# Optimization experiments

Measured on AMD Instinct MI355X. Metric: run time of the kernel, lower is better.

## Reference

```python
import jax, jax.numpy as jnp
import numpy as np

N = 64  # periodic element grid per side; nnode = N^3, ndof = 3*N^3
OFFSETS = [(0,0,0),(1,0,0),(0,1,0),(1,1,0),(0,0,1),(1,0,1),(0,1,1),(1,1,1)]


def setup_inputs() -> dict:
    key = jax.random.key(0)
    k1, k2, k3 = jax.random.split(key, 3)
    ndof = 3 * N ** 3
    U = jax.random.normal(k1, (ndof,), jnp.float32)
    rho = jax.random.uniform(k2, (N, N, N), jnp.float32)
    # nodIdx [nel, 8]: the 8 corner nodes of each element with periodic wrap
    idx = np.arange(N)
    I, J, K = np.meshgrid(idx, idx, idx, indexing='ij')
    cols = []
    for (di, dj, dk) in OFFSETS:
        n = (((I + di) % N) * N + (J + dj) % N) * N + (K + dk) % N
        cols.append(n.reshape(-1))
    nodIdx = jnp.asarray(np.stack(cols, axis=1), jnp.int32)  # [nel, 8]
    # 256 element stiffness matrices (24x24, symmetric), one per H8 type code
    filters = jax.random.normal(k3, (256, 24, 24), jnp.float32) * 0.05
    filters = 0.5 * (filters + filters.transpose(0, 2, 1))
    # typeFilter: 2x2x2 powers-of-two kernel encoding corner occupancy pattern
    typeFilter = jnp.asarray((2.0 ** np.arange(8)).reshape(2, 2, 2), jnp.float32)
    return {"U": U, "rho": rho, "nodIdx": nodIdx, "filters": filters, "typeFilter": typeFilter}


def _typeH8(rho, typeFilter):
    # binarize density and compute per-element type code via periodic 2x2x2 conv
    rb = (rho > 0.5).astype(rho.dtype)
    t = jnp.zeros_like(rho)
    for (di, dj, dk) in OFFSETS:
        t = t + typeFilter[di, dj, dk] * jnp.roll(rb, shift=(-di, -dj, -dk), axis=(0, 1, 2))
    return jax.lax.stop_gradient(t).astype(jnp.int32).reshape(-1)  # [nel] in 0..255


def reference(U, rho, nodIdx, filters, typeFilter):
    types = _typeH8(rho, typeFilter)                       # [nel]
    # dof indices per element: 8 nodes x 3 dofs, periodic wrap baked into nodIdx
    dofIdx = (nodIdx.astype(jnp.int32)[:, :, None] * 3 + jnp.arange(3, dtype=jnp.int32)).reshape(-1, 24)
    Ue = U[dofIdx]                                         # [nel, 24] gather
    Ke = filters[types]                                    # [nel, 24, 24] type-conditional filter select
    KUe = jnp.einsum('eij,ej->ei', Ke, Ue)                 # element-local stiffness apply
    KU = jnp.zeros_like(U).at[dofIdx.reshape(-1)].add(KUe.reshape(-1))  # scatter-add assembly
    return KU
```

## Files before the change

kernel.cpp:

```cpp
#include <hip/hip_runtime.h>
#include <hip/hip_fp16.h>

#define NGRID 64
#define NEL (NGRID*NGRID*NGRID)
#define IDX(i,j,k) ((((i)*64 + (j)) * 64) + (k))

#define NSLAB    16
#define SLAB_EL  16384
#define NTYPE    256
#define SLAB_PAD 32768
#define PADTOT   (NSLAB*SLAB_PAD)
#define NSLOT    (PADTOT/64)
#define SLAB_SLOTS (SLAB_PAD/64)

#define WS_U4     0
#define WS_KUE    (WS_U4 + (size_t)NEL*16)
#define WS_SORTED (WS_KUE + (size_t)NEL*64)
#define WS_TYPES  (WS_SORTED + (size_t)PADTOT*4)
#define WS_BHIST  (WS_TYPES + NEL)
#define WS_SLOT   (WS_BHIST + 4096*16*4)
#define WS_NEEDED (size_t)(WS_SLOT + NSLOT*4)

__device__ __forceinline__ int type_of(const float* __restrict__ rho, int i, int j, int k) {
    int i1 = (i + 1) & 63, j1 = (j + 1) & 63, k1 = (k + 1) & 63;
    int t = 0;
    t |= (rho[IDX(i,  j,  k )] > 0.5f ? 1 : 0) << 0;
    t |= (rho[IDX(i1, j,  k )] > 0.5f ? 1 : 0) << 4;
    t |= (rho[IDX(i,  j1, k )] > 0.5f ? 1 : 0) << 2;
    t |= (rho[IDX(i1, j1, k )] > 0.5f ? 1 : 0) << 6;
    t |= (rho[IDX(i,  j,  k1)] > 0.5f ? 1 : 0) << 1;
    t |= (rho[IDX(i1, j,  k1)] > 0.5f ? 1 : 0) << 5;
    t |= (rho[IDX(i,  j1, k1)] > 0.5f ? 1 : 0) << 3;
    t |= (rho[IDX(i1, j1, k1)] > 0.5f ? 1 : 0) << 7;
    return t;
}

__global__ __launch_bounds__(1024) void k1_hist(
    const float* __restrict__ U, const float* __restrict__ rho,
    float4* __restrict__ U4, unsigned char* __restrict__ types,
    int* __restrict__ bhist)
{
    __shared__ int lh[NTYPE];
    int tid = threadIdx.x;
    int b = blockIdx.x;
    int slab = b & 15, inner = b >> 4;
    if (tid < NTYPE) lh[tid] = 0;
    __syncthreads();

    int e = slab * SLAB_EL + inner * 1024 + tid;
    U4[e] = make_float4(U[3*e + 0], U[3*e + 1], U[3*e + 2], 0.0f);
    int k = e & 63, j = (e >> 6) & 63, i = (e >> 12) & 63;
    int t = type_of(rho, i, j, k);
    types[e] = (unsigned char)t;
    atomicAdd(&lh[t], 1);
    __syncthreads();
    if (tid < NTYPE) bhist[(slab * NTYPE + tid) * 16 + inner] = lh[tid];
}

__global__ __launch_bounds__(256) void k2_scan(
    int* __restrict__ bhist, int* __restrict__ slotinfo)
{
    int slab = blockIdx.x, t = threadIdx.x;
    int base = (slab * NTYPE + t) * 16;
    int c[16], sum = 0;
    #pragma unroll
    for (int in = 0; in < 16; ++in) { c[in] = bhist[base + in]; sum += c[in]; }
    int padded = (sum + 63) & ~63;

    __shared__ int s[256];
    __shared__ int used;
    s[t] = padded;
    __syncthreads();
    #pragma unroll
    for (int off = 1; off < 256; off <<= 1) {
        int tmp = (t >= off) ? s[t - off] : 0;
        __syncthreads();
        s[t] += tmp;
        __syncthreads();
    }
    int excl = s[t] - padded;
    int run = slab * SLAB_PAD + excl;
    #pragma unroll
    for (int in = 0; in < 16; ++in) { bhist[base + in] = run; run += c[in]; }

    int slot0 = slab * SLAB_SLOTS + (excl >> 6);
    int nslots = padded >> 6;
    for (int q = 0; q < nslots; ++q) {
        int cq = sum - (q << 6);
        cq = cq > 64 ? 64 : cq;
        slotinfo[slot0 + q] = (cq << 8) | t;
    }
    if (t == 255) used = s[255] >> 6;
    __syncthreads();
    for (int q = used + t; q < SLAB_SLOTS; q += 256)
        slotinfo[slab * SLAB_SLOTS + q] = 0;
}

__global__ __launch_bounds__(1024) void k3_scatter(
    const unsigned char* __restrict__ types, const int* __restrict__ bhist,
    int* __restrict__ sorted)
{
    __shared__ int lh[NTYPE];
    int tid = threadIdx.x;
    int b = blockIdx.x;
    int slab = b & 15, inner = b >> 4;
    if (tid < NTYPE) lh[tid] = 0;
    __syncthreads();
    int e = slab * SLAB_EL + inner * 1024 + tid;
    int t = types[e];
    int rank = atomicAdd(&lh[t], 1);
    int pos = bhist[(slab * NTYPE + t) * 16 + inner] + rank;
    sorted[pos] = e;
}

__global__ __launch_bounds__(256) void k4_apply(
    const float4* __restrict__ U4, const float* __restrict__ filters,
    const int* __restrict__ sorted, const int* __restrict__ slotinfo,
    float4* __restrict__ KUe16)
{
    int b = blockIdx.x;
    int hi = b >> 3;
    int slab = (b & 7) + 8 * (hi >> 7);
    int inner = hi & 127;
    int p = slab * SLAB_PAD + inner * 256 + threadIdx.x;

    int slot = __builtin_amdgcn_readfirstlane(p >> 6);
    int packed = slotinfo[slot];
    int t   = packed & 255;
    int cnt = packed >> 8;
    const float* __restrict__ F = filters + t * 576;

    if ((int)(threadIdx.x & 63) < cnt) {
        int e = sorted[p];
        int k = e & 63, j = (e >> 6) & 63, i = (e >> 12) & 63;
        int i1 = (i + 1) & 63, j1 = (j + 1) & 63, k1 = (k + 1) & 63;

        int nodes[8];
        nodes[0] = IDX(i,  j,  k );
        nodes[1] = IDX(i1, j,  k );
        nodes[2] = IDX(i,  j1, k );
        nodes[3] = IDX(i1, j1, k );
        nodes[4] = IDX(i,  j,  k1);
        nodes[5] = IDX(i1, j,  k1);
        nodes[6] = IDX(i,  j1, k1);
        nodes[7] = IDX(i1, j1, k1);

        float Ue[24];
        #pragma unroll
        for (int m = 0; m < 8; ++m) {
            float4 u = U4[nodes[m]];
            Ue[3*m + 0] = u.x;
            Ue[3*m + 1] = u.y;
            Ue[3*m + 2] = u.z;
        }

        float o[24];
        #pragma unroll
        for (int r = 0; r < 24; ++r) {
            float a = 0.0f;
            #pragma unroll
            for (int q = 0; q < 24; ++q)
                a = fmaf(F[r * 24 + q], Ue[q], a);
            o[r] = a;
        }

        union { __half2 h[16]; float4 f[4]; } ob;
        #pragma unroll
        for (int c = 0; c < 8; ++c) {
            ob.h[2*c + 0] = __floats2half2_rn(o[3*c + 0], o[3*c + 1]);
            ob.h[2*c + 1] = __floats2half2_rn(o[3*c + 2], 0.0f);
        }
        float4* __restrict__ dst = KUe16 + (size_t)e * 4;
        #pragma unroll
        for (int q = 0; q < 4; ++q) dst[q] = ob.f[q];
    }
}

__global__ __launch_bounds__(256) void k5_reduce(
    const uint2* __restrict__ KUe16, float* __restrict__ out)
{
    int b = blockIdx.x;
    int slab  = (b & 7) + 8 * (b >> 9);
    int chunk = (b >> 3) & 63;
    int n = slab * SLAB_EL + chunk * 256 + threadIdx.x;

    int k = n & 63, j = (n >> 6) & 63, i = (n >> 12) & 63;

    const int DI[8] = {0,1,0,1,0,1,0,1};
    const int DJ[8] = {0,0,1,1,0,0,1,1};
    const int DK[8] = {0,0,0,0,1,1,1,1};

    float a0 = 0.f, a1 = 0.f, a2 = 0.f;
    #pragma unroll
    for (int c = 0; c < 8; ++c) {
        int ei = (i - DI[c]) & 63;
        int ej = (j - DJ[c]) & 63;
        int ek = (k - DK[c]) & 63;
        uint2 v = KUe16[(size_t)IDX(ei, ej, ek) * 8 + c];
        union { unsigned u; __half2 h; } ux, uy;
        ux.u = v.x; uy.u = v.y;
        a0 += __low2float(ux.h);
        a1 += __high2float(ux.h);
        a2 += __low2float(uy.h);
    }
    out[n*3 + 0] = a0;
    out[n*3 + 1] = a1;
    out[n*3 + 2] = a2;
}

__global__ __launch_bounds__(256) void fe_apply_atomic(
    const float* __restrict__ U, const float* __restrict__ rho,
    const float* __restrict__ filters, float* __restrict__ out)
{
    int e = blockIdx.x * blockDim.x + threadIdx.x;
    int k = e & 63, j = (e >> 6) & 63, i = (e >> 12) & 63;
    int i1 = (i + 1) & 63, j1 = (j + 1) & 63, k1 = (k + 1) & 63;
    int nodes[8];
    nodes[0]=IDX(i,j,k);   nodes[1]=IDX(i1,j,k);   nodes[2]=IDX(i,j1,k);   nodes[3]=IDX(i1,j1,k);
    nodes[4]=IDX(i,j,k1);  nodes[5]=IDX(i1,j,k1);  nodes[6]=IDX(i,j1,k1);  nodes[7]=IDX(i1,j1,k1);
    int t = type_of(rho, i, j, k);
    float Ue[24];
    #pragma unroll
    for (int m = 0; m < 8; ++m) {
        int bb = nodes[m] * 3;
        Ue[3*m+0]=U[bb+0]; Ue[3*m+1]=U[bb+1]; Ue[3*m+2]=U[bb+2];
    }
    const float4* Kr = (const float4*)(filters + t * 576);
    #pragma unroll
    for (int r = 0; r < 24; ++r) {
        float a = 0.f;
        #pragma unroll
        for (int q = 0; q < 6; ++q) {
            float4 f = Kr[r*6+q];
            a = fmaf(f.x,Ue[4*q+0],a); a = fmaf(f.y,Ue[4*q+1],a);
            a = fmaf(f.z,Ue[4*q+2],a); a = fmaf(f.w,Ue[4*q+3],a);
        }
        atomicAdd(&out[nodes[r/3]*3 + (r%3)], a);
    }
}

extern "C" void kernel_launch(void* const* d_in, const int* in_sizes, int n_in,
                              void* d_out, int out_size, void* d_ws, size_t ws_size,
                              hipStream_t stream) {
    const float* U       = (const float*)d_in[0];
    const float* rho     = (const float*)d_in[1];
    const float* filters = (const float*)d_in[3];
    float* out = (float*)d_out;

    if (ws_size < WS_NEEDED) {
        hipMemsetAsync(out, 0, (size_t)out_size * sizeof(float), stream);
        fe_apply_atomic<<<dim3(NEL/256), dim3(256), 0, stream>>>(U, rho, filters, out);
        return;
    }

    char* ws = (char*)d_ws;
    float4*        U4     = (float4*)(ws + WS_U4);
    float4*        KUe16  = (float4*)(ws + WS_KUE);
    int*           sorted = (int*)(ws + WS_SORTED);
    unsigned char* types  = (unsigned char*)(ws + WS_TYPES);
    int*           bhist  = (int*)(ws + WS_BHIST);
    int*           slotinfo = (int*)(ws + WS_SLOT);

    k1_hist   <<<dim3(256),  dim3(1024), 0, stream>>>(U, rho, U4, types, bhist);
    k2_scan   <<<dim3(16),   dim3(256),  0, stream>>>(bhist, slotinfo);
    k3_scatter<<<dim3(256),  dim3(1024), 0, stream>>>(types, bhist, sorted);
    k4_apply  <<<dim3(2048), dim3(256),  0, stream>>>(U4, filters, sorted, slotinfo, KUe16);
    k5_reduce <<<dim3(1024), dim3(256),  0, stream>>>((const uint2*)KUe16, out);
}
```

Measured before the change: 40.06 us.

## Fuse scan into scatter kernel and stage reduce inputs through LDS tiles

The separate per-slab scan kernel is folded into the scatter kernel. Each block now recomputes the 256-type prefix scan redundantly, and only inner==0 blocks write slotinfo, which removes one launch and a global round-trip through bhist. The reduce kernel now uses 1024-thread blocks that cooperatively load a 2x17x64 element halo of KUe16 into about 139KB of dynamic LDS with coalesced 16-byte reads, then gather the 8 corner contributions from shared memory. The cost is redundant scan work, a large LDS footprint that limits occupancy to one block per CU, and a per-call hipFuncSetAttribute call.

After: 38.09 us. 4.9% less time.

```diff
diff --git a/kernel.cpp b/kernel.cpp
--- a/kernel.cpp
+++ b/kernel.cpp
@@ -12,6 +12,9 @@
 #define PADTOT   (NSLAB*SLAB_PAD)
 #define NSLOT    (PADTOT/64)
 #define SLAB_SLOTS (SLAB_PAD/64)
+
+#define STAGE_EL 2176
+#define K5_LDS   (8*STAGE_EL*8)
 
 #define WS_U4     0
 #define WS_KUE    (WS_U4 + (size_t)NEL*16)
@@ -46,7 +49,6 @@
     int slab = b & 15, inner = b >> 4;
     if (tid < NTYPE) lh[tid] = 0;
     __syncthreads();
-
     int e = slab * SLAB_EL + inner * 1024 + tid;
     U4[e] = make_float4(U[3*e + 0], U[3*e + 1], U[3*e + 2], 0.0f);
     int k = e & 63, j = (e >> 6) & 63, i = (e >> 12) & 63;
@@ -57,60 +59,62 @@
     if (tid < NTYPE) bhist[(slab * NTYPE + tid) * 16 + inner] = lh[tid];
 }
 
-__global__ __launch_bounds__(256) void k2_scan(
-    int* __restrict__ bhist, int* __restrict__ slotinfo)
-{
-    int slab = blockIdx.x, t = threadIdx.x;
-    int base = (slab * NTYPE + t) * 16;
-    int c[16], sum = 0;
-    #pragma unroll
-    for (int in = 0; in < 16; ++in) { c[in] = bhist[base + in]; sum += c[in]; }
-    int padded = (sum + 63) & ~63;
-
-    __shared__ int s[256];
+__global__ __launch_bounds__(1024) void k3_scan_scatter(
+    const unsigned char* __restrict__ types, const int* __restrict__ bhist,
+    int* __restrict__ sorted, int* __restrict__ slotinfo)
+{
+    __shared__ int s[NTYPE];
+    __shared__ int off[NTYPE];
+    __shared__ int lh[NTYPE];
     __shared__ int used;
-    s[t] = padded;
-    __syncthreads();
-    #pragma unroll
-    for (int off = 1; off < 256; off <<= 1) {
-        int tmp = (t >= off) ? s[t - off] : 0;
+    int tid = threadIdx.x;
+    int b = blockIdx.x;
+    int slab = b & 15, inner = b >> 4;
+
+    int c[16], sum = 0, before = 0, padded = 0;
+    if (tid < NTYPE) {
+        lh[tid] = 0;
+        int base = (slab * NTYPE + tid) * 16;
+        #pragma unroll
+        for (int in = 0; in < 16; ++in) {
+            c[in] = bhist[base + in];
+            if (in < inner) before += c[in];
+            sum += c[in];
+        }
+        padded = (sum + 63) & ~63;
+        s[tid] = padded;
+    }
+    __syncthreads();
+    #pragma unroll
+    for (int o = 1; o < NTYPE; o <<= 1) {
+        int tmp = (tid < NTYPE && tid >= o) ? s[tid - o] : 0;
         __syncthreads();
-        s[t] += tmp;
+        if (tid < NTYPE) s[tid] += tmp;
         __syncthreads();
     }
-    int excl = s[t] - padded;
-    int run = slab * SLAB_PAD + excl;
-    #pragma unroll
-    for (int in = 0; in < 16; ++in) { bhist[base + in] = run; run += c[in]; }
-
-    int slot0 = slab * SLAB_SLOTS + (excl >> 6);
-    int nslots = padded >> 6;
-    for (int q = 0; q < nslots; ++q) {
-        int cq = sum - (q << 6);
-        cq = cq > 64 ? 64 : cq;
-        slotinfo[slot0 + q] = (cq << 8) | t;
-    }
-    if (t == 255) used = s[255] >> 6;
-    __syncthreads();
-    for (int q = used + t; q < SLAB_SLOTS; q += 256)
-        slotinfo[slab * SLAB_SLOTS + q] = 0;
-}
-
-__global__ __launch_bounds__(1024) void k3_scatter(
-    const unsigned char* __restrict__ types, const int* __restrict__ bhist,
-    int* __restrict__ sorted)
-{
-    __shared__ int lh[NTYPE];
-    int tid = threadIdx.x;
-    int b = blockIdx.x;
-    int slab = b & 15, inner = b >> 4;
-    if (tid < NTYPE) lh[tid] = 0;
-    __syncthreads();
+    if (tid < NTYPE) {
+        int excl = s[tid] - padded;
+        off[tid] = slab * SLAB_PAD + excl + before;
+        if (inner == 0) {
+            int slot0 = slab * SLAB_SLOTS + (excl >> 6);
+            int nslots = padded >> 6;
+            for (int q = 0; q < nslots; ++q) {
+                int cq = sum - (q << 6);
+                cq = cq > 64 ? 64 : cq;
+                slotinfo[slot0 + q] = (cq << 8) | tid;
+            }
+            if (tid == 255) used = s[255] >> 6;
+        }
+    }
+    __syncthreads();
+    if (inner == 0) {
+        for (int q = used + tid; q < SLAB_SLOTS; q += 1024)
+            slotinfo[slab * SLAB_SLOTS + q] = 0;
+    }
     int e = slab * SLAB_EL + inner * 1024 + tid;
     int t = types[e];
     int rank = atomicAdd(&lh[t], 1);
-    int pos = bhist[(slab * NTYPE + t) * 16 + inner] + rank;
-    sorted[pos] = e;
+    sorted[off[t] + rank] = e;
 }
 
 __global__ __launch_bounds__(256) void k4_apply(
@@ -134,7 +138,6 @@
         int e = sorted[p];
         int k = e & 63, j = (e >> 6) & 63, i = (e >> 12) & 63;
         int i1 = (i + 1) & 63, j1 = (j + 1) & 63, k1 = (k + 1) & 63;
-
         int nodes[8];
         nodes[0] = IDX(i,  j,  k );
         nodes[1] = IDX(i1, j,  k );
@@ -144,7 +147,6 @@
         nodes[5] = IDX(i1, j,  k1);
         nodes[6] = IDX(i,  j1, k1);
         nodes[7] = IDX(i1, j1, k1);
-
         float Ue[24];
         #pragma unroll
         for (int m = 0; m < 8; ++m) {
@@ -153,7 +155,6 @@
             Ue[3*m + 1] = u.y;
             Ue[3*m + 2] = u.z;
         }
-
         float o[24];
         #pragma unroll
         for (int r = 0; r < 24; ++r) {
@@ -163,7 +164,6 @@
                 a = fmaf(F[r * 24 + q], Ue[q], a);
             o[r] = a;
         }
-
         union { __half2 h[16]; float4 f[4]; } ob;
         #pragma unroll
         for (int c = 0; c < 8; ++c) {
@@ -176,27 +176,43 @@
     }
 }
 
-__global__ __launch_bounds__(256) void k5_reduce(
-    const uint2* __restrict__ KUe16, float* __restrict__ out)
-{
-    int b = blockIdx.x;
-    int slab  = (b & 7) + 8 * (b >> 9);
-    int chunk = (b >> 3) & 63;
-    int n = slab * SLAB_EL + chunk * 256 + threadIdx.x;
-
-    int k = n & 63, j = (n >> 6) & 63, i = (n >> 12) & 63;
-
+__global__ __launch_bounds__(1024) void k5_reduce(
+    const uint4* __restrict__ KUe4, float* __restrict__ out)
+{
+    extern __shared__ uint2 cache[];
+    int tid = threadIdx.x;
+    int b = blockIdx.x;
+    int slab  = (b & 7) + 8 * (b >> 7);
+    int inner = (b >> 3) & 15;
+    int i  = slab * 4 + (inner >> 2);
+    int j0 = (inner & 3) << 4;
+    int im1 = (i - 1) & 63;
+
+    for (int f = tid; f < STAGE_EL * 4; f += 1024) {
+        int le = f >> 2, s = f & 3;
+        int pi = (le >= 1088) ? 1 : 0;
+        int rem = le - pi * 1088;
+        int pj = rem >> 6, ek = rem & 63;
+        int ei = pi ? i : im1;
+        int ej = (j0 - 1 + pj) & 63;
+        uint4 v = KUe4[(size_t)IDX(ei, ej, ek) * 4 + s];
+        cache[(2*s)     * STAGE_EL + le] = make_uint2(v.x, v.y);
+        cache[(2*s + 1) * STAGE_EL + le] = make_uint2(v.z, v.w);
+    }
+    __syncthreads();
+
+    int jj = tid >> 6, k = tid & 63;
+    int n = IDX(i, j0 + jj, k);
     const int DI[8] = {0,1,0,1,0,1,0,1};
     const int DJ[8] = {0,0,1,1,0,0,1,1};
     const int DK[8] = {0,0,0,0,1,1,1,1};
-
     float a0 = 0.f, a1 = 0.f, a2 = 0.f;
     #pragma unroll
     for (int c = 0; c < 8; ++c) {
-        int ei = (i - DI[c]) & 63;
-        int ej = (j - DJ[c]) & 63;
+        int pi = 1 - DI[c];
+        int pj = jj + 1 - DJ[c];
         int ek = (k - DK[c]) & 63;
-        uint2 v = KUe16[(size_t)IDX(ei, ej, ek) * 8 + c];
+        uint2 v = cache[c * STAGE_EL + pi * 1088 + pj * 64 + ek];
         union { unsigned u; __half2 h; } ux, uy;
         ux.u = v.x; uy.u = v.y;
         a0 += __low2float(ux.h);
@@ -254,16 +270,18 @@
     }
 
     char* ws = (char*)d_ws;
-    float4*        U4     = (float4*)(ws + WS_U4);
-    float4*        KUe16  = (float4*)(ws + WS_KUE);
-    int*           sorted = (int*)(ws + WS_SORTED);
-    unsigned char* types  = (unsigned char*)(ws + WS_TYPES);
-    int*           bhist  = (int*)(ws + WS_BHIST);
+    float4*        U4       = (float4*)(ws + WS_U4);
+    float4*        KUe16    = (float4*)(ws + WS_KUE);
+    int*           sorted   = (int*)(ws + WS_SORTED);
+    unsigned char* types    = (unsigned char*)(ws + WS_TYPES);
+    int*           bhist    = (int*)(ws + WS_BHIST);
     int*           slotinfo = (int*)(ws + WS_SLOT);
 
-    k1_hist   <<<dim3(256),  dim3(1024), 0, stream>>>(U, rho, U4, types, bhist);
-    k2_scan   <<<dim3(16),   dim3(256),  0, stream>>>(bhist, slotinfo);
-    k3_scatter<<<dim3(256),  dim3(1024), 0, stream>>>(types, bhist, sorted);
-    k4_apply  <<<dim3(2048), dim3(256),  0, stream>>>(U4, filters, sorted, slotinfo, KUe16);
-    k5_reduce <<<dim3(1024), dim3(256),  0, stream>>>((const uint2*)KUe16, out);
-}
+    (void)hipFuncSetAttribute((const void*)k5_reduce,
+                              hipFuncAttributeMaxDynamicSharedMemorySize, K5_LDS);
+
+    k1_hist        <<<dim3(256),  dim3(1024), 0,      stream>>>(U, rho, U4, types, bhist);
+    k3_scan_scatter<<<dim3(256),  dim3(1024), 0,      stream>>>(types, bhist, sorted, slotinfo);
+    k4_apply       <<<dim3(2048), dim3(256),  0,      stream>>>(U4, filters, sorted, slotinfo, KUe16);
+    k5_reduce      <<<dim3(256),  dim3(1024), K5_LDS, stream>>>((const uint4*)KUe16, out);
+}
```
